# Optimization experiments

Measured on AMD Instinct MI355X. Metric: run time of the kernel, lower is better.

## Reference

```python
import jax, jax.numpy as jnp
import numpy as np

V, E, NH, HS, FF, NB, L = 16, 512, 8, 64, 2048, 6, 512  # NB = num_layers + 2
B, T = 16, 512
TEMP = 1.0 * 0.8


def layer_norm(x, g, b, eps=1e-5):
    mu = jnp.mean(x, axis=-1, keepdims=True)
    var = jnp.mean(jnp.square(x - mu), axis=-1, keepdims=True)
    return (x - mu) * jax.lax.rsqrt(var + eps) * g + b


def setup_inputs() -> dict:
    key = jax.random.key(0)
    ks = iter(jax.random.split(key, 32))
    s = 0.02
    d = {
        'x': jax.random.randint(next(ks), (B, T), 0, V),
        'emb': jax.random.normal(next(ks), (V, E), jnp.float32) * s,
        'pos': jax.random.normal(next(ks), (L, E), jnp.float32) * s,
        'wq': jax.random.normal(next(ks), (NB, NH, E, HS), jnp.float32) * s,
        'wk': jax.random.normal(next(ks), (NB, NH, E, HS), jnp.float32) * s,
        'wv': jax.random.normal(next(ks), (NB, NH, E, HS), jnp.float32) * s,
        'proj_w': jax.random.normal(next(ks), (NB, NH * HS, E), jnp.float32) * s,
        'proj_b': jnp.zeros((NB, E), jnp.float32),
        'ln1_g': jnp.ones((NB, E), jnp.float32),
        'ln1_b': jnp.zeros((NB, E), jnp.float32),
        'ln2_g': jnp.ones((NB, E), jnp.float32),
        'ln2_b': jnp.zeros((NB, E), jnp.float32),
        'ff_w1': jax.random.normal(next(ks), (NB, E, FF), jnp.float32) * s,
        'ff_b1': jnp.zeros((NB, FF), jnp.float32),
        'ff_w2': jax.random.normal(next(ks), (NB, FF, E), jnp.float32) * s,
        'ff_b2': jnp.zeros((NB, E), jnp.float32),
        'lnf_g': jnp.ones((E,), jnp.float32),
        'lnf_b': jnp.zeros((E,), jnp.float32),
        'out_w': jax.random.normal(next(ks), (E, V), jnp.float32) * s,
        'out_b': jnp.zeros((V,), jnp.float32),
    }
    return d


def reference(x, emb, pos, wq, wk, wv, proj_w, proj_b, ln1_g, ln1_b, ln2_g, ln2_b,
              ff_w1, ff_b1, ff_w2, ff_b2, lnf_g, lnf_b, out_w, out_b):
    Bv, Tv = x.shape
    # Abacus embedding: token + (clamped) position embedding
    positions = jnp.minimum(jnp.arange(Tv), L - 1)
    h = emb[x] + pos[positions][None, :, :]  # [B,T,E]

    causal = jnp.tril(jnp.ones((Tv, Tv), bool))  # True = attend
    scale = HS ** -0.5

    for i in range(NB):
        # multi-head causal self-attention (all heads batched)
        xn = layer_norm(h, ln1_g[i], ln1_b[i])
        q = jnp.einsum('bte,hed->bhtd', xn, wq[i])
        k = jnp.einsum('bte,hed->bhtd', xn, wk[i])
        v = jnp.einsum('bte,hed->bhtd', xn, wv[i])
        scores = jnp.einsum('bhqd,bhkd->bhqk', q, k) * scale
        scores = jnp.where(causal[None, None], scores, -jnp.inf)
        attn = jax.nn.softmax(scores, axis=-1)
        o = jnp.einsum('bhqk,bhkd->bhqd', attn, v)
        o = o.transpose(0, 2, 1, 3).reshape(Bv, Tv, NH * HS)
        h = h + o @ proj_w[i] + proj_b[i]
        # FFN
        xn = layer_norm(h, ln2_g[i], ln2_b[i])
        h = h + jax.nn.relu(xn @ ff_w1[i] + ff_b1[i]) @ ff_w2[i] + ff_b2[i]

    h = layer_norm(h, lnf_g, lnf_b)
    logits = (h @ out_w + out_b) / TEMP
    return logits
```

## Files before the change

kernel.cpp:

```cpp
#include <hip/hip_runtime.h>
#include <hip/hip_bf16.h>

typedef __bf16 bf16;
typedef __bf16 bf16x8 __attribute__((ext_vector_type(8)));
typedef float f32x4 __attribute__((ext_vector_type(4)));

#define NB_ 6
#define E_ 512
#define NH_ 8
#define HS_ 64
#define FF_ 2048
#define B_ 16
#define T_ 512
#define M_ 8192

#define SW(r) (((r) ^ ((r) >> 3)) & 7)

typedef const __attribute__((address_space(1))) void* gptr_t;
typedef __attribute__((address_space(3))) void* sptr_t;

__global__ __launch_bounds__(256) void conv_qkv_tiled(
    const float* __restrict__ wq, const float* __restrict__ wk,
    const float* __restrict__ wv, bf16* __restrict__ dst)
{
    __shared__ float tile[32][65];
    const int e0 = blockIdx.x * 32;
    const int wh = blockIdx.y;
    const int which = wh >> 3, h = wh & 7;
    const int i = blockIdx.z;
    const float* src = (which == 0) ? wq : (which == 1) ? wk : wv;
    src += (((size_t)i * NH_ + h) * E_ + e0) * HS_;
    const int d = threadIdx.x & 63, er = threadIdx.x >> 6;
#pragma unroll
    for (int j = 0; j < 32; j += 4)
        tile[j + er][d] = src[(size_t)(j + er) * HS_ + d];
    __syncthreads();
    const int e = threadIdx.x & 31, dr = threadIdx.x >> 5;
    bf16* dbase = dst + (size_t)i * 1536 * E_ + ((size_t)which * 512 + h * 64) * E_ + e0;
#pragma unroll
    for (int j = 0; j < 64; j += 8)
        dbase[(size_t)(j + dr) * E_ + e] = (bf16)tile[e][j + dr];
}

__global__ __launch_bounds__(256) void transpose_tiled(
    const float* __restrict__ src, bf16* __restrict__ dst, int K, int N)
{
    __shared__ float tile[32][33];
    const int n0 = blockIdx.x * 32, k0 = blockIdx.y * 32;
    const size_t sb = (size_t)blockIdx.z * K * N;
    const int lx = threadIdx.x & 31, ly = threadIdx.x >> 5;
#pragma unroll
    for (int j = 0; j < 32; j += 8)
        tile[j + ly][lx] = src[sb + (size_t)(k0 + j + ly) * N + n0 + lx];
    __syncthreads();
#pragma unroll
    for (int j = 0; j < 32; j += 8)
        dst[sb + (size_t)(n0 + j + ly) * K + k0 + lx] = (bf16)tile[lx][j + ly];
}

__global__ __launch_bounds__(256) void embed_kernel(
    const int* __restrict__ x, const float* __restrict__ emb,
    const float* __restrict__ pos, float* __restrict__ h)
{
    int idx = blockIdx.x * 256 + threadIdx.x;
    int row = idx >> 7;
    int e4 = (idx & 127) << 2;
    int tok = x[row];
    int t = row & (T_ - 1);
    float4 a = *(const float4*)&emb[(size_t)tok * E_ + e4];
    float4 c = *(const float4*)&pos[(size_t)t * E_ + e4];
    float4 o; o.x = a.x + c.x; o.y = a.y + c.y; o.z = a.z + c.z; o.w = a.w + c.w;
    *(float4*)&h[(size_t)row * E_ + e4] = o;
}

template<int OUT_F32>
__global__ __launch_bounds__(256) void ln_kernel(
    const float* __restrict__ x, const float* __restrict__ gw,
    const float* __restrict__ bw, void* __restrict__ out)
{
    int wave = threadIdx.x >> 6, lane = threadIdx.x & 63;
    int row = blockIdx.x * 4 + wave;
    const float* xr = x + (size_t)row * E_;
    float4 v0 = *(const float4*)&xr[lane * 8];
    float4 v1 = *(const float4*)&xr[lane * 8 + 4];
    float vals[8] = {v0.x, v0.y, v0.z, v0.w, v1.x, v1.y, v1.z, v1.w};
    float s = 0.f, ss = 0.f;
#pragma unroll
    for (int j = 0; j < 8; ++j) { s += vals[j]; ss += vals[j] * vals[j]; }
#pragma unroll
    for (int m = 1; m < 64; m <<= 1) { s += __shfl_xor(s, m, 64); ss += __shfl_xor(ss, m, 64); }
    float mu = s * (1.f / E_);
    float var = ss * (1.f / E_) - mu * mu;
    float rs = rsqrtf(var + 1e-5f);
    int e0 = lane * 8;
    if (OUT_F32) {
        float* o = (float*)out + (size_t)row * E_ + e0;
#pragma unroll
        for (int j = 0; j < 8; ++j) o[j] = (vals[j] - mu) * rs * gw[e0 + j] + bw[e0 + j];
    } else {
        bf16x8 o;
#pragma unroll
        for (int j = 0; j < 8; ++j) o[j] = (bf16)((vals[j] - mu) * rs * gw[e0 + j] + bw[e0 + j]);
        *(bf16x8*)&((bf16*)out)[(size_t)row * E_ + e0] = o;
    }
}

template<int BN_T, int HAS_BIAS, int HAS_RES, int RELU, int OUT_BF16>
__global__ __launch_bounds__(256) void gemm_bt(
    const bf16* __restrict__ A, const bf16* __restrict__ Bt,
    const float* __restrict__ bias, const float* __restrict__ res,
    void* __restrict__ out, int M, int N, int K)
{
    constexpr int BM = 128, BK = 64;
    constexpr int NI = BN_T / 32;
    __shared__ bf16 As[BM * BK];
    __shared__ bf16 Bs[BN_T * BK];
    const int tid = threadIdx.x;
    const int wave = tid >> 6, lane = tid & 63;
    const int l15 = lane & 15, g = lane >> 4;
    const int m0 = blockIdx.x * BM, n0 = blockIdx.y * BN_T;
    const int wm = (wave >> 1) * 64, wn = (wave & 1) * (BN_T / 2);
    const int sr = tid >> 3, sc = tid & 7;
    f32x4 acc[4][NI] = {};
    for (int k0 = 0; k0 < K; k0 += BK) {
        __syncthreads();
#pragma unroll
        for (int p = 0; p < 4; ++p) {
            int row = p * 32 + sr;
            int cg = sc ^ SW(row);
            __builtin_amdgcn_global_load_lds(
                (gptr_t)&A[(size_t)(m0 + row) * K + k0 + cg * 8],
                (sptr_t)&As[row * 64 + sc * 8], 16, 0, 0);
        }
#pragma unroll
        for (int p = 0; p < BN_T / 32; ++p) {
            int row = p * 32 + sr;
            int cg = sc ^ SW(row);
            __builtin_amdgcn_global_load_lds(
                (gptr_t)&Bt[(size_t)(n0 + row) * K + k0 + cg * 8],
                (sptr_t)&Bs[row * 64 + sc * 8], 16, 0, 0);
        }
        __syncthreads();
#pragma unroll
        for (int kk = 0; kk < 2; ++kk) {
            bf16x8 af[4], bg[NI];
#pragma unroll
            for (int mi = 0; mi < 4; ++mi) {
                int row = wm + 16 * mi + l15;
                af[mi] = *(const bf16x8*)&As[row * 64 + ((kk * 4 + g) ^ SW(row)) * 8];
            }
#pragma unroll
            for (int ni = 0; ni < NI; ++ni) {
                int row = wn + 16 * ni + l15;
                bg[ni] = *(const bf16x8*)&Bs[row * 64 + ((kk * 4 + g) ^ SW(row)) * 8];
            }
#pragma unroll
            for (int mi = 0; mi < 4; ++mi)
#pragma unroll
                for (int ni = 0; ni < NI; ++ni)
                    acc[mi][ni] = __builtin_amdgcn_mfma_f32_16x16x32_bf16(
                        af[mi], bg[ni], acc[mi][ni], 0, 0, 0);
        }
    }
#pragma unroll
    for (int mi = 0; mi < 4; ++mi) {
#pragma unroll
        for (int ni = 0; ni < NI; ++ni) {
#pragma unroll
            for (int r = 0; r < 4; ++r) {
                int rr = m0 + wm + 16 * mi + 4 * g + r;
                int cc = n0 + wn + 16 * ni + l15;
                float v = acc[mi][ni][r];
                if (HAS_BIAS) v += bias[cc];
                if (HAS_RES) v += res[(size_t)rr * N + cc];
                if (RELU) v = fmaxf(v, 0.f);
                if (OUT_BF16) ((bf16*)out)[(size_t)rr * N + cc] = (bf16)v;
                else ((float*)out)[(size_t)rr * N + cc] = v;
            }
        }
    }
}

__global__ __launch_bounds__(256) void attn_kernel(
    const bf16* __restrict__ qkv, bf16* __restrict__ out)
{
    constexpr int RS = 3 * E_;
    __shared__ bf16 Ks[64 * 64];
    __shared__ bf16 Vt[64 * 64];
    __shared__ bf16 Ps[4][16 * 64];
    const int tid = threadIdx.x;
    const int wave = tid >> 6, lane = tid & 63;
    const int l15 = lane & 15, g = lane >> 4;
    const int bh = blockIdx.x;
    const int b = bh >> 3, h = bh & 7;
    const size_t base = (size_t)b * T_ * RS;
    const bf16* kb = qkv + base + E_ + h * HS_;
    const bf16* vb = qkv + base + 2 * E_ + h * HS_;
    const int strow = tid >> 3, stc = tid & 7;

    for (int half = 0; half < 2; ++half) {
        const int qt = half == 0 ? (int)blockIdx.y : 7 - (int)blockIdx.y;
        const int q0 = qt * 64;
        const int ntiles = qt + 1;
        bf16x8 qf[2];
        {
            const bf16* qrow = qkv + base + (size_t)(q0 + wave * 16 + l15) * RS + h * HS_;
            qf[0] = *(const bf16x8*)&qrow[8 * g];
            qf[1] = *(const bf16x8*)&qrow[32 + 8 * g];
        }
        float mrow[4] = {-1e30f, -1e30f, -1e30f, -1e30f};
        float lrow[4] = {0.f, 0.f, 0.f, 0.f};
        f32x4 accO[4] = {};
        bf16x8 kreg[2], vreg[2];
#pragma unroll
        for (int r = 0; r < 2; ++r) {
            int krow = r * 32 + strow;
            kreg[r] = *(const bf16x8*)&kb[(size_t)krow * RS + stc * 8];
            vreg[r] = *(const bf16x8*)&vb[(size_t)krow * RS + stc * 8];
        }
        for (int tile = 0; tile < ntiles; ++tile) {
            __syncthreads();
#pragma unroll
            for (int r = 0; r < 2; ++r) {
                int krow = r * 32 + strow;
                *(bf16x8*)&Ks[krow * 64 + (stc ^ SW(krow)) * 8] = kreg[r];
#pragma unroll
                for (int j = 0; j < 8; ++j) {
                    int drow = stc * 8 + j;
                    Vt[drow * 64 + ((krow >> 3) ^ SW(drow)) * 8 + (krow & 7)] = vreg[r][j];
                }
            }
            if (tile + 1 < ntiles) {
                int kv = (tile + 1) * 64;
#pragma unroll
                for (int r = 0; r < 2; ++r) {
                    int krow = kv + r * 32 + strow;
                    kreg[r] = *(const bf16x8*)&kb[(size_t)krow * RS + stc * 8];
                    vreg[r] = *(const bf16x8*)&vb[(size_t)krow * RS + stc * 8];
                }
            }
            __syncthreads();
            f32x4 accS[4] = {};
#pragma unroll
            for (int t = 0; t < 4; ++t) {
                int rk = 16 * t + l15;
#pragma unroll
                for (int kc = 0; kc < 2; ++kc) {
                    bf16x8 kf = *(const bf16x8*)&Ks[rk * 64 + ((kc * 4 + g) ^ SW(rk)) * 8];
                    accS[t] = __builtin_amdgcn_mfma_f32_16x16x32_bf16(qf[kc], kf, accS[t], 0, 0, 0);
                }
            }
            float sarr[4][4];
            const bool diag = (tile == qt);
#pragma unroll
            for (int t = 0; t < 4; ++t)
#pragma unroll
                for (int r = 0; r < 4; ++r) {
                    float s = accS[t][r] * 0.125f;
                    if (diag && (16 * t + l15 > 16 * wave + 4 * g + r)) s = -1e30f;
                    sarr[t][r] = s;
                }
            float alpha[4];
#pragma unroll
            for (int r = 0; r < 4; ++r) {
                float mx = fmaxf(fmaxf(sarr[0][r], sarr[1][r]), fmaxf(sarr[2][r], sarr[3][r]));
#pragma unroll
                for (int m = 1; m < 16; m <<= 1) mx = fmaxf(mx, __shfl_xor(mx, m, 64));
                float mnew = fmaxf(mrow[r], mx);
                alpha[r] = __expf(mrow[r] - mnew);
                mrow[r] = mnew;
            }
#pragma unroll
            for (int t = 0; t < 4; ++t)
#pragma unroll
                for (int r = 0; r < 4; ++r) sarr[t][r] = __expf(sarr[t][r] - mrow[r]);
#pragma unroll
            for (int r = 0; r < 4; ++r) {
                float rs0 = sarr[0][r] + sarr[1][r] + sarr[2][r] + sarr[3][r];
#pragma unroll
                for (int m = 1; m < 16; m <<= 1) rs0 += __shfl_xor(rs0, m, 64);
                lrow[r] = lrow[r] * alpha[r] + rs0;
            }
#pragma unroll
            for (int u = 0; u < 4; ++u)
#pragma unroll
                for (int r = 0; r < 4; ++r) accO[u][r] *= alpha[r];
#pragma unroll
            for (int t = 0; t < 4; ++t)
#pragma unroll
                for (int r = 0; r < 4; ++r) {
                    int prow = 4 * g + r;
                    Ps[wave][prow * 64 + ((2 * t + (l15 >> 3)) ^ SW(prow)) * 8 + (l15 & 7)] =
                        (bf16)sarr[t][r];
                }
#pragma unroll
            for (int kc = 0; kc < 2; ++kc) {
                bf16x8 pf = *(const bf16x8*)&Ps[wave][l15 * 64 + ((kc * 4 + g) ^ SW(l15)) * 8];
#pragma unroll
                for (int u = 0; u < 4; ++u) {
                    int rv = 16 * u + l15;
                    bf16x8 vf = *(const bf16x8*)&Vt[rv * 64 + ((kc * 4 + g) ^ SW(rv)) * 8];
                    accO[u] = __builtin_amdgcn_mfma_f32_16x16x32_bf16(pf, vf, accO[u], 0, 0, 0);
                }
            }
        }
#pragma unroll
        for (int u = 0; u < 4; ++u)
#pragma unroll
            for (int r = 0; r < 4; ++r) {
                int row = q0 + 16 * wave + 4 * g + r;
                out[((size_t)b * T_ + row) * E_ + h * HS_ + 16 * u + l15] =
                    (bf16)(accO[u][r] / lrow[r]);
            }
    }
}

__global__ __launch_bounds__(256) void outproj_kernel(
    const float* __restrict__ hn, const float* __restrict__ W,
    const float* __restrict__ bias, float* __restrict__ out)
{
    int idx = blockIdx.x * 256 + threadIdx.x;
    int row = idx >> 4, v = idx & 15;
    const float* hr = hn + (size_t)row * E_;
    float acc = 0.f;
#pragma unroll 8
    for (int k = 0; k < E_; ++k) acc += hr[k] * W[k * 16 + v];
    out[idx] = (acc + bias[v]) * 1.25f;
}

extern "C" void kernel_launch(void* const* d_in, const int* in_sizes, int n_in,
                              void* d_out, int out_size, void* d_ws, size_t ws_size,
                              hipStream_t stream)
{
    const int*   x      = (const int*)d_in[0];
    const float* emb    = (const float*)d_in[1];
    const float* pos    = (const float*)d_in[2];
    const float* wq     = (const float*)d_in[3];
    const float* wk     = (const float*)d_in[4];
    const float* wv     = (const float*)d_in[5];
    const float* proj_w = (const float*)d_in[6];
    const float* proj_b = (const float*)d_in[7];
    const float* ln1_g  = (const float*)d_in[8];
    const float* ln1_b  = (const float*)d_in[9];
    const float* ln2_g  = (const float*)d_in[10];
    const float* ln2_b  = (const float*)d_in[11];
    const float* ff_w1  = (const float*)d_in[12];
    const float* ff_b1  = (const float*)d_in[13];
    const float* ff_w2  = (const float*)d_in[14];
    const float* ff_b2  = (const float*)d_in[15];
    const float* lnf_g  = (const float*)d_in[16];
    const float* lnf_b  = (const float*)d_in[17];
    const float* out_w  = (const float*)d_in[18];
    const float* out_b  = (const float*)d_in[19];

    char* ws = (char*)d_ws;
    size_t off = 0;
    auto alloc = [&](size_t bytes) { size_t r = off; off += (bytes + 255) & ~(size_t)255; return r; };
    bf16*  wqkv_t = (bf16*)(ws + alloc((size_t)NB_ * 1536 * 512 * 2));
    bf16*  projt  = (bf16*)(ws + alloc((size_t)NB_ * 512 * 512 * 2));
    bf16*  ff1t   = (bf16*)(ws + alloc((size_t)NB_ * 2048 * 512 * 2));
    bf16*  ff2t   = (bf16*)(ws + alloc((size_t)NB_ * 512 * 2048 * 2));
    float* h      = (float*)(ws + alloc((size_t)M_ * 512 * 4));
    bf16*  xn     = (bf16*)(ws + alloc((size_t)M_ * 512 * 2));
    bf16*  qkvb   = (bf16*)(ws + alloc((size_t)M_ * 1536 * 2));
    bf16*  aout   = (bf16*)(ws + alloc((size_t)M_ * 512 * 2));
    bf16*  ffact  = (bf16*)(ws + alloc((size_t)M_ * 2048 * 2));
    float* hn     = (float*)(ws + alloc((size_t)M_ * 512 * 4));
    (void)ws_size; (void)in_sizes; (void)n_in; (void)out_size;

    conv_qkv_tiled<<<dim3(16, 24, NB_), 256, 0, stream>>>(wq, wk, wv, wqkv_t);
    transpose_tiled<<<dim3(512 / 32, 512 / 32, NB_), 256, 0, stream>>>(proj_w, projt, 512, 512);
    transpose_tiled<<<dim3(2048 / 32, 512 / 32, NB_), 256, 0, stream>>>(ff_w1, ff1t, 512, 2048);
    transpose_tiled<<<dim3(512 / 32, 2048 / 32, NB_), 256, 0, stream>>>(ff_w2, ff2t, 2048, 512);

    embed_kernel<<<(M_ * 128) / 256, 256, 0, stream>>>(x, emb, pos, h);

    for (int i = 0; i < NB_; ++i) {
        ln_kernel<0><<<M_ / 4, 256, 0, stream>>>(h, ln1_g + i * 512, ln1_b + i * 512, xn);
        gemm_bt<128, 0, 0, 0, 1><<<dim3(M_ / 128, 1536 / 128), 256, 0, stream>>>(
            xn, wqkv_t + (size_t)i * 1536 * 512, nullptr, nullptr, qkvb, M_, 1536, 512);
        attn_kernel<<<dim3(B_ * NH_, 4), 256, 0, stream>>>(qkvb, aout);
        gemm_bt<64, 1, 1, 0, 0><<<dim3(M_ / 128, 512 / 64), 256, 0, stream>>>(
            aout, projt + (size_t)i * 512 * 512, proj_b + i * 512, h, h, M_, 512, 512);
        ln_kernel<0><<<M_ / 4, 256, 0, stream>>>(h, ln2_g + i * 512, ln2_b + i * 512, xn);
        gemm_bt<128, 1, 0, 1, 1><<<dim3(M_ / 128, 2048 / 128), 256, 0, stream>>>(
            xn, ff1t + (size_t)i * 2048 * 512, ff_b1 + i * 2048, nullptr, ffact, M_, 2048, 512);
        gemm_bt<64, 1, 1, 0, 0><<<dim3(M_ / 128, 512 / 64), 256, 0, stream>>>(
            ffact, ff2t + (size_t)i * 512 * 2048, ff_b2 + i * 512, h, h, M_, 512, 2048);
    }
    ln_kernel<1><<<M_ / 4, 256, 0, stream>>>(h, lnf_g, lnf_b, hn);
    outproj_kernel<<<(M_ * 16) / 256, 256, 0, stream>>>(hn, out_w, out_b, (float*)d_out);
}
```

Baseline: 937.1 us.

## Double-buffer LDS tiles in gemm_bt for BN=64 to overlap loads with MFMA

For the BN_T=64 instantiation, the GEMM now keeps two LDS buffers and issues the global-to-LDS loads for the next K tile before computing the current one. A partial s_waitcnt vmcnt(6) waits only for the previous stage's loads, since each stage issues 6 loads per thread. The aim is to hide global memory latency behind MFMA work instead of serializing load, barrier, then compute. It doubles LDS use for that variant, which may lower occupancy, and it relies on a hand-counted vmcnt value being correct.

```diff
diff --git a/kernel.cpp b/kernel.cpp
--- a/kernel.cpp
+++ b/kernel.cpp
@@ -113,8 +113,10 @@
 {
     constexpr int BM = 128, BK = 64;
     constexpr int NI = BN_T / 32;
-    __shared__ bf16 As[BM * BK];
-    __shared__ bf16 Bs[BN_T * BK];
+    constexpr bool DBUF = (BN_T == 64);
+    constexpr int NBUF = DBUF ? 2 : 1;
+    __shared__ bf16 As[NBUF][BM * BK];
+    __shared__ bf16 Bs[NBUF][BN_T * BK];
     const int tid = threadIdx.x;
     const int wave = tid >> 6, lane = tid & 63;
     const int l15 = lane & 15, g = lane >> 4;
@@ -122,15 +124,15 @@
     const int wm = (wave >> 1) * 64, wn = (wave & 1) * (BN_T / 2);
     const int sr = tid >> 3, sc = tid & 7;
     f32x4 acc[4][NI] = {};
-    for (int k0 = 0; k0 < K; k0 += BK) {
-        __syncthreads();
+
+    auto stage = [&](int buf, int k0) {
 #pragma unroll
         for (int p = 0; p < 4; ++p) {
             int row = p * 32 + sr;
             int cg = sc ^ SW(row);
             __builtin_amdgcn_global_load_lds(
                 (gptr_t)&A[(size_t)(m0 + row) * K + k0 + cg * 8],
-                (sptr_t)&As[row * 64 + sc * 8], 16, 0, 0);
+                (sptr_t)&As[buf][row * 64 + sc * 8], 16, 0, 0);
         }
 #pragma unroll
         for (int p = 0; p < BN_T / 32; ++p) {
@@ -138,21 +140,22 @@
             int cg = sc ^ SW(row);
             __builtin_amdgcn_global_load_lds(
                 (gptr_t)&Bt[(size_t)(n0 + row) * K + k0 + cg * 8],
-                (sptr_t)&Bs[row * 64 + sc * 8], 16, 0, 0);
-        }
-        __syncthreads();
+                (sptr_t)&Bs[buf][row * 64 + sc * 8], 16, 0, 0);
+        }
+    };
+    auto compute = [&](int buf) {
 #pragma unroll
         for (int kk = 0; kk < 2; ++kk) {
             bf16x8 af[4], bg[NI];
 #pragma unroll
             for (int mi = 0; mi < 4; ++mi) {
                 int row = wm + 16 * mi + l15;
-                af[mi] = *(const bf16x8*)&As[row * 64 + ((kk * 4 + g) ^ SW(row)) * 8];
+                af[mi] = *(const bf16x8*)&As[buf][row * 64 + ((kk * 4 + g) ^ SW(row)) * 8];
             }
 #pragma unroll
             for (int ni = 0; ni < NI; ++ni) {
                 int row = wn + 16 * ni + l15;
-                bg[ni] = *(const bf16x8*)&Bs[row * 64 + ((kk * 4 + g) ^ SW(row)) * 8];
+                bg[ni] = *(const bf16x8*)&Bs[buf][row * 64 + ((kk * 4 + g) ^ SW(row)) * 8];
             }
 #pragma unroll
             for (int mi = 0; mi < 4; ++mi)
@@ -161,7 +164,34 @@
                     acc[mi][ni] = __builtin_amdgcn_mfma_f32_16x16x32_bf16(
                         af[mi], bg[ni], acc[mi][ni], 0, 0, 0);
         }
+    };
+
+    if constexpr (DBUF) {
+        const int nt = K / BK;
+        stage(0, 0);
+        int cur = 0;
+        for (int t = 0; t < nt; ++t) {
+            if (t + 1 < nt) {
+                stage(cur ^ 1, (t + 1) * BK);
+                asm volatile("s_waitcnt vmcnt(6)" ::: "memory");
+            } else {
+                asm volatile("s_waitcnt vmcnt(0)" ::: "memory");
+            }
+            __builtin_amdgcn_s_barrier();
+            compute(cur);
+            __builtin_amdgcn_s_barrier();
+            asm volatile("" ::: "memory");
+            cur ^= 1;
+        }
+    } else {
+        for (int k0 = 0; k0 < K; k0 += BK) {
+            __syncthreads();
+            stage(0, k0);
+            __syncthreads();
+            compute(0);
+        }
     }
+
 #pragma unroll
     for (int mi = 0; mi < 4; ++mi) {
 #pragma unroll
```

Result: faster. 915.1 us (-2.3%).
